# Optimization experiments

Measured on AMD Instinct MI355X. Metric: run time of the kernel, lower is better.

Reference implementation:

```python
import jax, jax.numpy as jnp
import numpy as np

NUM_HEADS = 16
HIDDEN = 1024
HEAD = HIDDEN // NUM_HEADS


def setup_inputs() -> dict:
    key = jax.random.key(0)
    k1, k2, k3, k4, k5 = jax.random.split(key, 5)
    b, s, d = 2, 2048, HIDDEN
    scale = 1.0 / np.sqrt(d)
    return {
        "features": jax.random.normal(k1, (b, s, d), dtype=jnp.float32),
        "qkv_w": jax.random.normal(k2, (3 * d, d), dtype=jnp.float32) * scale,  # torch Linear weight [out,in]
        "qkv_b": jax.random.normal(k3, (3 * d,), dtype=jnp.float32) * 0.01,
        "out_w": jax.random.normal(k4, (d, d), dtype=jnp.float32) * scale,
        "out_b": jax.random.normal(k5, (d,), dtype=jnp.float32) * 0.01,
        "use_causal_mask": 0,
    }


def reference(features, qkv_w, qkv_b, out_w, out_b, use_causal_mask):
    b, s, d = features.shape
    qkv = features @ qkv_w.T + qkv_b                      # [b,s,3d]
    q, k, v = jnp.split(qkv, 3, axis=-1)
    # [b,s,d] -> [b,h,s,hd]
    def heads(x):
        return x.reshape(b, s, NUM_HEADS, HEAD).transpose(0, 2, 1, 3)
    q, k, v = heads(q), heads(k), heads(v)
    scores = jnp.einsum("bhqd,bhkd->bhqk", q, k) / np.sqrt(HEAD)
    if use_causal_mask:
        mask = jnp.triu(jnp.ones((s, s), dtype=bool), k=1)
        scores = jnp.where(mask, -jnp.inf, scores)
    attn = jax.nn.softmax(scores, axis=-1)
    out = jnp.einsum("bhqk,bhkd->bhqd", attn, v)          # [b,h,s,hd]
    out = out.transpose(0, 2, 1, 3).reshape(b, s, d)
    return out @ out_w.T + out_b
```

## Files before the change

kernel.cpp:

```cpp
#include <hip/hip_runtime.h>
#include <hip/hip_bf16.h>
#include <math.h>

#define BATCH 2
#define SEQ   2048
#define HID   1024
#define NHEAD 16
#define ROWS  (BATCH*SEQ)
#define QKV_N (3*HID)

#define Q_SCALE 0.18033688011112042f

typedef __attribute__((ext_vector_type(8))) short bf16x8;
typedef __attribute__((ext_vector_type(4))) float f32x4;

__device__ __forceinline__ unsigned short f2b(float f) {
    unsigned u = __float_as_uint(f);
    u += 0x7FFF + ((u >> 16) & 1);
    return (unsigned short)(u >> 16);
}
__device__ __forceinline__ unsigned pk2c(float a, float b) {
    __hip_bfloat162 h = __float22bfloat162_rn(float2{a, b});
    union { __hip_bfloat162 h2; unsigned u; } cv; cv.h2 = h;
    return cv.u;
}

#define GLOAD_LDS16(gp, lp) \
    __builtin_amdgcn_global_load_lds((const __attribute__((address_space(1))) void*)(gp), \
                                     (__attribute__((address_space(3))) void*)(lp), 16, 0, 0)

__global__ __launch_bounds__(256)
void cvt_all(const float* __restrict__ a, unsigned short* __restrict__ oa, int na4,
             const float* __restrict__ b, unsigned short* __restrict__ ob, int nb4,
             const float* __restrict__ c, unsigned short* __restrict__ oc, int nc4) {
    int i = blockIdx.x * 256 + threadIdx.x;
    const float* src; unsigned short* dst; int j;
    if (i < na4)            { src = a; dst = oa; j = i; }
    else if (i < na4 + nb4) { src = b; dst = ob; j = i - na4; }
    else if (i < na4 + nb4 + nc4) { src = c; dst = oc; j = i - na4 - nb4; }
    else return;
    float4 v = reinterpret_cast<const float4*>(src)[j];
    ushort4 o;
    o.x = f2b(v.x); o.y = f2b(v.y); o.z = f2b(v.z); o.w = f2b(v.w);
    reinterpret_cast<ushort4*>(dst)[j] = o;
}

template<int MODE>
__global__ __launch_bounds__(256)
void gemm_mfma(const unsigned short* __restrict__ A, const unsigned short* __restrict__ B,
               const float* __restrict__ bias, void* __restrict__ Cout,
               unsigned short* __restrict__ vt, int M, int N, int K) {
    __shared__ __align__(16) unsigned short As[128 * 32];
    __shared__ __align__(16) unsigned short Bs[128 * 32];
    const int tid = threadIdx.x;
    const int w = tid >> 6, l = tid & 63;
    const int wm = w >> 1, wn = w & 1;
    const int l15 = l & 15, l4 = l >> 4;
    const long row0 = (long)blockIdx.y * 128;
    const long col0 = (long)blockIdx.x * 128;

    f32x4 acc[4][4];
    #pragma unroll
    for (int m = 0; m < 4; ++m)
        #pragma unroll
        for (int n = 0; n < 4; ++n) acc[m][n] = (f32x4)0.0f;

    const int lr   = l >> 2;
    const int slot = (l & 3) ^ (lr & 3);

    for (int k0 = 0; k0 < K; k0 += 32) {
        __syncthreads();
        #pragma unroll
        for (int c = 0; c < 2; ++c) {
            int r = w * 32 + c * 16 + lr;
            GLOAD_LDS16(A + (row0 + r) * K + k0 + slot * 8, As + (w * 32 + c * 16) * 32);
            GLOAD_LDS16(B + (col0 + r) * K + k0 + slot * 8, Bs + (w * 32 + c * 16) * 32);
        }
        __syncthreads();

        bf16x8 af[4], bfr[4];
        #pragma unroll
        for (int m = 0; m < 4; ++m) {
            int row = wm * 64 + m * 16 + l15;
            af[m] = *(const bf16x8*)((const char*)As + row * 64 + ((l4 ^ (row & 3)) << 4));
        }
        #pragma unroll
        for (int n = 0; n < 4; ++n) {
            int row = wn * 64 + n * 16 + l15;
            bfr[n] = *(const bf16x8*)((const char*)Bs + row * 64 + ((l4 ^ (row & 3)) << 4));
        }
        #pragma unroll
        for (int m = 0; m < 4; ++m)
            #pragma unroll
            for (int n = 0; n < 4; ++n)
                acc[m][n] = __builtin_amdgcn_mfma_f32_16x16x32_bf16(af[m], bfr[n], acc[m][n], 0, 0, 0);
    }

    #pragma unroll
    for (int m = 0; m < 4; ++m) {
        #pragma unroll
        for (int n = 0; n < 4; ++n) {
            long ccol = col0 + wn * 64 + n * 16 + l15;
            float bv = bias[ccol];
            #pragma unroll
            for (int r2 = 0; r2 < 4; ++r2) {
                long crow = row0 + wm * 64 + m * 16 + l4 * 4 + r2;
                float v = acc[m][n][r2] + bv;
                if (MODE == 0) {
                    ((float*)Cout)[crow * N + ccol] = v;
                } else {
                    if (ccol < 1024) {
                        ((unsigned short*)Cout)[crow * QKV_N + ccol] = f2b(v * Q_SCALE);
                    } else if (ccol < 2048) {
                        ((unsigned short*)Cout)[crow * QKV_N + ccol] = f2b(v);
                    } else {
                        long cc = ccol - 2048;
                        long h = cc >> 6, d = cc & 63;
                        long b = crow >> 11, s = crow & 2047;
                        vt[(((b * NHEAD + h) * 64 + d) << 11) + s] = f2b(v);
                    }
                }
            }
        }
    }
}

__global__ __launch_bounds__(256, 4)
void attn_mfma(const unsigned short* __restrict__ qkv, const unsigned short* __restrict__ vt,
               unsigned short* __restrict__ attno, const int* __restrict__ use_mask) {
    __shared__ __align__(16) unsigned short Ks [64 * 64];
    __shared__ __align__(16) unsigned short Vts[64 * 64];
    __shared__ __align__(16) unsigned short Ps [4][32 * 32];
    const int tid = threadIdx.x;
    const int w = tid >> 6, l = tid & 63;
    const int l15 = l & 15, l4 = l >> 4;
    const int bid  = blockIdx.x;
    const int orig = (bid & 7) * 128 + (bid >> 3);
    const int qt = orig & 31, bh = orig >> 5;
    const int b = bh >> 4, h = bh & 15;
    const int q0 = qt * 64;
    const int qh = w & 1, kh = w >> 1;
    const int wq0 = q0 + qh * 32;
    const int causal = use_mask[0];
    const int NT = causal ? (qt + 1) : (SEQ / 64);

    bf16x8 qf[2][2];
    #pragma unroll
    for (int m = 0; m < 2; ++m) {
        const unsigned short* qp = qkv + (size_t)(b * SEQ + wq0 + m * 16 + l15) * QKV_N + h * 64;
        qf[m][0] = *(const bf16x8*)(qp + l4 * 8);
        qf[m][1] = *(const bf16x8*)(qp + 32 + l4 * 8);
    }

    f32x4 o_acc[2][4];
    #pragma unroll
    for (int m = 0; m < 2; ++m)
        #pragma unroll
        for (int n = 0; n < 4; ++n) o_acc[m][n] = (f32x4)0.0f;
    f32x4 l_acc[2] = {(f32x4)0.0f, (f32x4)0.0f};

    bf16x8 ones;
    #pragma unroll
    for (int j = 0; j < 8; ++j) ones[j] = (short)0x3F80;

    const int srow = l >> 3, g = l & 7;
    const int r0   = w * 16 + srow;
    const int wso  = (g ^ srow) << 3;
    unsigned short* pw = Ps[w];

    const unsigned short* kp = qkv + (size_t)b * SEQ * QKV_N + HID + h * 64
                                   + (size_t)r0 * QKV_N + g * 8;
    const unsigned short* vp = vt + (size_t)bh * 64 * SEQ + (size_t)r0 * SEQ + g * 8;

    bf16x8 kreg[2], vreg[2];
    kreg[0] = *(const bf16x8*)(kp);
    kreg[1] = *(const bf16x8*)(kp + 8 * QKV_N);
    vreg[0] = *(const bf16x8*)(vp);
    vreg[1] = *(const bf16x8*)(vp + 8 * SEQ);
    kp += (size_t)64 * QKV_N;
    vp += 64;

    for (int kt = 0; kt < NT; ++kt) {
        __syncthreads();
        #pragma unroll
        for (int c = 0; c < 2; ++c) {
            *(bf16x8*)(Ks  + (r0 + c * 8) * 64 + wso) = kreg[c];
            *(bf16x8*)(Vts + (r0 + c * 8) * 64 + wso) = vreg[c];
        }
        __syncthreads();

        if (kt + 1 < NT) {
            kreg[0] = *(const bf16x8*)(kp);
            kreg[1] = *(const bf16x8*)(kp + 8 * QKV_N);
            vreg[0] = *(const bf16x8*)(vp);
            vreg[1] = *(const bf16x8*)(vp + 8 * SEQ);
            kp += (size_t)64 * QKV_N;
            vp += 64;
        }

        f32x4 s_acc[2][2];
        #pragma unroll
        for (int n2 = 0; n2 < 2; ++n2)
            #pragma unroll
            for (int m = 0; m < 2; ++m) s_acc[n2][m] = (f32x4)0.0f;
        __builtin_amdgcn_s_setprio(1);
        #pragma unroll
        for (int ks = 0; ks < 2; ++ks) {
            #pragma unroll
            for (int n2 = 0; n2 < 2; ++n2) {
                int row = kh * 32 + n2 * 16 + l15;
                bf16x8 kf = *(const bf16x8*)((const char*)Ks + row * 128 + (((ks * 4 + l4) ^ (row & 7)) << 4));
                #pragma unroll
                for (int m = 0; m < 2; ++m)
                    s_acc[n2][m] = __builtin_amdgcn_mfma_f32_16x16x32_bf16(kf, qf[m][ks], s_acc[n2][m], 0, 0, 0);
            }
        }
        __builtin_amdgcn_s_setprio(0);

        if (causal) {
            int kk0 = kt * 64 + kh * 32;
            #pragma unroll
            for (int n2 = 0; n2 < 2; ++n2)
                #pragma unroll
                for (int m = 0; m < 2; ++m)
                    #pragma unroll
                    for (int r2 = 0; r2 < 4; ++r2) {
                        int krow = kk0 + n2 * 16 + l4 * 4 + r2;
                        int qcol = wq0 + m * 16 + l15;
                        if (krow > qcol) s_acc[n2][m][r2] = -INFINITY;
                    }
        }

        #pragma unroll
        for (int m = 0; m < 2; ++m) {
            int prow = m * 16 + l15;
            #pragma unroll
            for (int n2 = 0; n2 < 2; ++n2) {
                float p0 = exp2f(s_acc[n2][m][0]);
                float p1 = exp2f(s_acc[n2][m][1]);
                float p2 = exp2f(s_acc[n2][m][2]);
                float p3 = exp2f(s_acc[n2][m][3]);
                uint2 pk;
                pk.x = pk2c(p0, p1);
                pk.y = pk2c(p2, p3);
                int byteoff = (n2 * 32 + l4 * 8) ^ ((prow & 3) << 4);
                *(uint2*)((char*)pw + prow * 64 + byteoff) = pk;
            }
        }

        __builtin_amdgcn_s_setprio(1);
        bf16x8 pf[2];
        #pragma unroll
        for (int m = 0; m < 2; ++m) {
            int prow = m * 16 + l15;
            pf[m] = *(const bf16x8*)((const char*)pw + prow * 64 + ((l4 * 16) ^ ((prow & 3) << 4)));
            l_acc[m] = __builtin_amdgcn_mfma_f32_16x16x32_bf16(pf[m], ones, l_acc[m], 0, 0, 0);
        }
        #pragma unroll
        for (int n = 0; n < 4; ++n) {
            int vrow = n * 16 + l15;
            bf16x8 vf = *(const bf16x8*)((const char*)Vts + vrow * 128 + (((kh * 4 + l4) ^ (vrow & 7)) << 4));
            #pragma unroll
            for (int m = 0; m < 2; ++m)
                o_acc[m][n] = __builtin_amdgcn_mfma_f32_16x16x32_bf16(pf[m], vf, o_acc[m][n], 0, 0, 0);
        }
        __builtin_amdgcn_s_setprio(0);
    }

    __syncthreads();
    float* mq = (float*)(qh ? Vts : Ks);
    float* lb = (float*)&Ps[0][0];
    if (kh == 1) {
        #pragma unroll
        for (int m = 0; m < 2; ++m) {
            #pragma unroll
            for (int r2 = 0; r2 < 4; ++r2) {
                int qr = m * 16 + l4 * 4 + r2;
                #pragma unroll
                for (int n = 0; n < 4; ++n)
                    mq[qr * 64 + n * 16 + l15] = o_acc[m][n][r2];
                if (l15 == 0) lb[qh * 32 + qr] = l_acc[m][r2];
            }
        }
    }
    __syncthreads();
    if (kh == 0) {
        #pragma unroll
        for (int m = 0; m < 2; ++m) {
            #pragma unroll
            for (int r2 = 0; r2 < 4; ++r2) {
                int qr = m * 16 + l4 * 4 + r2;
                float lt = l_acc[m][r2] + lb[qh * 32 + qr];
                float inv = 1.0f / lt;
                size_t orow = (size_t)(b * SEQ + wq0 + qr);
                #pragma unroll
                for (int n = 0; n < 4; ++n) {
                    float o = o_acc[m][n][r2] + mq[qr * 64 + n * 16 + l15];
                    attno[orow * HID + h * 64 + n * 16 + l15] = f2b(o * inv);
                }
            }
        }
    }
}

extern "C" void kernel_launch(void* const* d_in, const int* in_sizes, int n_in,
                              void* d_out, int out_size, void* d_ws, size_t ws_size,
                              hipStream_t stream) {
    const float* features = (const float*)d_in[0];
    const float* qkv_w    = (const float*)d_in[1];
    const float* qkv_b    = (const float*)d_in[2];
    const float* out_w    = (const float*)d_in[3];
    const float* out_b    = (const float*)d_in[4];
    const int*   use_mask = (const int*)d_in[5];

    char* ws = (char*)d_ws;
    unsigned short* fbf     = (unsigned short*)(ws);
    unsigned short* wbf     = (unsigned short*)(ws + 8388608);
    unsigned short* owbf    = (unsigned short*)(ws + 14680064);
    unsigned short* qkvbf   = (unsigned short*)(ws + 16777216);
    unsigned short* vtbuf   = (unsigned short*)(ws + 41943040);
    unsigned short* attnobf = (unsigned short*)(ws + 50331648);

    cvt_all<<<8192, 256, 0, stream>>>(features, fbf, 1048576,
                                      qkv_w, wbf, 786432,
                                      out_w, owbf, 262144);

    dim3 g1(QKV_N / 128, ROWS / 128);
    gemm_mfma<2><<<g1, 256, 0, stream>>>(fbf, wbf, qkv_b, (void*)qkvbf, vtbuf,
                                         ROWS, QKV_N, HID);

    attn_mfma<<<1024, 256, 0, stream>>>(qkvbf, vtbuf, attnobf, use_mask);

    dim3 g3(HID / 128, ROWS / 128);
    gemm_mfma<0><<<g3, 256, 0, stream>>>(attnobf, owbf, out_b, d_out, (unsigned short*)nullptr,
                                         ROWS, HID, HID);
}
```

Before: 148.4 us.

## Compute V transposed via separate swapped-operand GEMM and pad P LDS rows

The QKV projection is split in two. One GEMM produces Q and K in a 2048-wide row-major buffer. A second GEMM computes V^T directly by swapping the operands (W_v as A, features as B) and adding the bias per row. This replaces the scattered strided transposed stores of V in the old epilogue with contiguous stores, at the cost of an extra kernel launch. The per-wave P scratch in LDS also switches from an XOR swizzle to an 80-byte padded row stride to avoid bank conflicts with simpler addressing.

New measurement: 157.0 us. 5.8% more time.

```diff
diff --git a/kernel.cpp b/kernel.cpp
--- a/kernel.cpp
+++ b/kernel.cpp
@@ -7,7 +7,8 @@
 #define HID   1024
 #define NHEAD 16
 #define ROWS  (BATCH*SEQ)
-#define QKV_N (3*HID)
+#define QK_N  2048
+#define VT_N  (BATCH*SEQ)
 
 #define Q_SCALE 0.18033688011112042f
 
@@ -49,7 +50,7 @@
 __global__ __launch_bounds__(256)
 void gemm_mfma(const unsigned short* __restrict__ A, const unsigned short* __restrict__ B,
                const float* __restrict__ bias, void* __restrict__ Cout,
-               unsigned short* __restrict__ vt, int M, int N, int K) {
+               int M, int N, int K) {
     __shared__ __align__(16) unsigned short As[128 * 32];
     __shared__ __align__(16) unsigned short Bs[128 * 32];
     const int tid = threadIdx.x;
@@ -101,24 +102,19 @@
         #pragma unroll
         for (int n = 0; n < 4; ++n) {
             long ccol = col0 + wn * 64 + n * 16 + l15;
-            float bv = bias[ccol];
+            float bvc = (MODE != 1) ? bias[ccol] : 0.0f;
             #pragma unroll
             for (int r2 = 0; r2 < 4; ++r2) {
                 long crow = row0 + wm * 64 + m * 16 + l4 * 4 + r2;
-                float v = acc[m][n][r2] + bv;
                 if (MODE == 0) {
-                    ((float*)Cout)[crow * N + ccol] = v;
+                    ((float*)Cout)[crow * N + ccol] = acc[m][n][r2] + bvc;
+                } else if (MODE == 2) {
+                    float v = acc[m][n][r2] + bvc;
+                    ((unsigned short*)Cout)[crow * QK_N + ccol] =
+                        (ccol < 1024) ? f2b(v * Q_SCALE) : f2b(v);
                 } else {
-                    if (ccol < 1024) {
-                        ((unsigned short*)Cout)[crow * QKV_N + ccol] = f2b(v * Q_SCALE);
-                    } else if (ccol < 2048) {
-                        ((unsigned short*)Cout)[crow * QKV_N + ccol] = f2b(v);
-                    } else {
-                        long cc = ccol - 2048;
-                        long h = cc >> 6, d = cc & 63;
-                        long b = crow >> 11, s = crow & 2047;
-                        vt[(((b * NHEAD + h) * 64 + d) << 11) + s] = f2b(v);
-                    }
+                    float v = acc[m][n][r2] + bias[crow];
+                    ((unsigned short*)Cout)[crow * N + ccol] = f2b(v);
                 }
             }
         }
@@ -126,11 +122,11 @@
 }
 
 __global__ __launch_bounds__(256, 4)
-void attn_mfma(const unsigned short* __restrict__ qkv, const unsigned short* __restrict__ vt,
+void attn_mfma(const unsigned short* __restrict__ qk, const unsigned short* __restrict__ vtD,
                unsigned short* __restrict__ attno, const int* __restrict__ use_mask) {
     __shared__ __align__(16) unsigned short Ks [64 * 64];
     __shared__ __align__(16) unsigned short Vts[64 * 64];
-    __shared__ __align__(16) unsigned short Ps [4][32 * 32];
+    __shared__ __align__(16) unsigned short Ps [4][32 * 40];
     const int tid = threadIdx.x;
     const int w = tid >> 6, l = tid & 63;
     const int l15 = l & 15, l4 = l >> 4;
@@ -147,7 +143,7 @@
     bf16x8 qf[2][2];
     #pragma unroll
     for (int m = 0; m < 2; ++m) {
-        const unsigned short* qp = qkv + (size_t)(b * SEQ + wq0 + m * 16 + l15) * QKV_N + h * 64;
+        const unsigned short* qp = qk + (size_t)(b * SEQ + wq0 + m * 16 + l15) * QK_N + h * 64;
         qf[m][0] = *(const bf16x8*)(qp + l4 * 8);
         qf[m][1] = *(const bf16x8*)(qp + 32 + l4 * 8);
     }
@@ -168,16 +164,16 @@
     const int wso  = (g ^ srow) << 3;
     unsigned short* pw = Ps[w];
 
-    const unsigned short* kp = qkv + (size_t)b * SEQ * QKV_N + HID + h * 64
-                                   + (size_t)r0 * QKV_N + g * 8;
-    const unsigned short* vp = vt + (size_t)bh * 64 * SEQ + (size_t)r0 * SEQ + g * 8;
+    const unsigned short* kp = qk + (size_t)b * SEQ * QK_N + 1024 + h * 64
+                                  + (size_t)r0 * QK_N + g * 8;
+    const unsigned short* vp = vtD + (size_t)(h * 64 + r0) * VT_N + b * SEQ + g * 8;
 
     bf16x8 kreg[2], vreg[2];
     kreg[0] = *(const bf16x8*)(kp);
-    kreg[1] = *(const bf16x8*)(kp + 8 * QKV_N);
+    kreg[1] = *(const bf16x8*)(kp + 8 * QK_N);
     vreg[0] = *(const bf16x8*)(vp);
-    vreg[1] = *(const bf16x8*)(vp + 8 * SEQ);
-    kp += (size_t)64 * QKV_N;
+    vreg[1] = *(const bf16x8*)(vp + 8 * VT_N);
+    kp += (size_t)64 * QK_N;
     vp += 64;
 
     for (int kt = 0; kt < NT; ++kt) {
@@ -191,10 +187,10 @@
 
         if (kt + 1 < NT) {
             kreg[0] = *(const bf16x8*)(kp);
-            kreg[1] = *(const bf16x8*)(kp + 8 * QKV_N);
+            kreg[1] = *(const bf16x8*)(kp + 8 * QK_N);
             vreg[0] = *(const bf16x8*)(vp);
-            vreg[1] = *(const bf16x8*)(vp + 8 * SEQ);
-            kp += (size_t)64 * QKV_N;
+            vreg[1] = *(const bf16x8*)(vp + 8 * VT_N);
+            kp += (size_t)64 * QK_N;
             vp += 64;
         }
 
@@ -243,8 +239,7 @@
                 uint2 pk;
                 pk.x = pk2c(p0, p1);
                 pk.y = pk2c(p2, p3);
-                int byteoff = (n2 * 32 + l4 * 8) ^ ((prow & 3) << 4);
-                *(uint2*)((char*)pw + prow * 64 + byteoff) = pk;
+                *(uint2*)((char*)pw + prow * 80 + n2 * 32 + l4 * 8) = pk;
             }
         }
 
@@ -253,7 +248,7 @@
         #pragma unroll
         for (int m = 0; m < 2; ++m) {
             int prow = m * 16 + l15;
-            pf[m] = *(const bf16x8*)((const char*)pw + prow * 64 + ((l4 * 16) ^ ((prow & 3) << 4)));
+            pf[m] = *(const bf16x8*)((const char*)pw + prow * 80 + l4 * 16);
             l_acc[m] = __builtin_amdgcn_mfma_f32_16x16x32_bf16(pf[m], ones, l_acc[m], 0, 0, 0);
         }
         #pragma unroll
@@ -317,21 +312,24 @@
     unsigned short* fbf     = (unsigned short*)(ws);
     unsigned short* wbf     = (unsigned short*)(ws + 8388608);
     unsigned short* owbf    = (unsigned short*)(ws + 14680064);
-    unsigned short* qkvbf   = (unsigned short*)(ws + 16777216);
-    unsigned short* vtbuf   = (unsigned short*)(ws + 41943040);
-    unsigned short* attnobf = (unsigned short*)(ws + 50331648);
+    unsigned short* qkbf    = (unsigned short*)(ws + 16777216);
+    unsigned short* vtD     = (unsigned short*)(ws + 33554432);
+    unsigned short* attnobf = (unsigned short*)(ws + 41943040);
 
     cvt_all<<<8192, 256, 0, stream>>>(features, fbf, 1048576,
                                       qkv_w, wbf, 786432,
                                       out_w, owbf, 262144);
 
-    dim3 g1(QKV_N / 128, ROWS / 128);
-    gemm_mfma<2><<<g1, 256, 0, stream>>>(fbf, wbf, qkv_b, (void*)qkvbf, vtbuf,
-                                         ROWS, QKV_N, HID);
-
-    attn_mfma<<<1024, 256, 0, stream>>>(qkvbf, vtbuf, attnobf, use_mask);
+    dim3 g1(QK_N / 128, ROWS / 128);
+    gemm_mfma<2><<<g1, 256, 0, stream>>>(fbf, wbf, qkv_b, (void*)qkbf,
+                                         ROWS, QK_N, HID);
+    dim3 gv(VT_N / 128, 1024 / 128);
+    gemm_mfma<1><<<gv, 256, 0, stream>>>(wbf + 2048 * 1024, fbf, qkv_b + 2048, (void*)vtD,
+                                         1024, VT_N, HID);
+
+    attn_mfma<<<1024, 256, 0, stream>>>(qkbf, vtD, attnobf, use_mask);
 
     dim3 g3(HID / 128, ROWS / 128);
-    gemm_mfma<0><<<g3, 256, 0, stream>>>(attnobf, owbf, out_b, d_out, (unsigned short*)nullptr,
+    gemm_mfma<0><<<g3, 256, 0, stream>>>(attnobf, owbf, out_b, d_out,
                                          ROWS, HID, HID);
 }
```
